# Performance work log

Hardware: AMD Instinct MI355X
Metric: run time of the kernel (lower is better)

## Reference

```python
import jax, jax.numpy as jnp
import numpy as np

N_EMBD = 1024
N_HEAD = 16

def setup_inputs() -> dict:
    key = jax.random.key(0)
    k1, k2, k3, k4, k5 = jax.random.split(key, 5)
    C = N_EMBD
    s = 1.0 / np.sqrt(C)
    return {
        "x": jax.random.normal(k1, (2, 2048, C), dtype=jnp.float32),
        "W_attn": jax.random.normal(k2, (C, 3 * C), dtype=jnp.float32) * s,
        "b_attn": jax.random.normal(k3, (3 * C,), dtype=jnp.float32) * 0.02,
        "W_proj": jax.random.normal(k4, (C, C), dtype=jnp.float32) * s,
        "b_proj": jax.random.normal(k5, (C,), dtype=jnp.float32) * 0.02,
    }

def reference(x, W_attn, b_attn, W_proj, b_proj):
    B, T, C = x.shape
    nh = N_HEAD
    hs = C // nh
    qkv = x @ W_attn + b_attn                      # [B, T, 3C]
    q, k, v = jnp.split(qkv, 3, axis=-1)
    # [B, T, C] -> [B, nh, T, hs]
    def to_heads(t):
        return t.reshape(B, T, nh, hs).transpose(0, 2, 1, 3)
    q, k, v = to_heads(q), to_heads(k), to_heads(v)
    scale = 1.0 / np.sqrt(hs).astype(np.float32)
    att = jnp.einsum('bhqd,bhkd->bhqk', q, k) * scale   # [B, nh, T, T]
    causal = jnp.tril(jnp.ones((T, T), dtype=bool))
    att = jnp.where(causal, att, -jnp.inf)
    att = jax.nn.softmax(att, axis=-1)
    y = jnp.einsum('bhqk,bhkd->bhqd', att, v)           # [B, nh, T, hs]
    y = y.transpose(0, 2, 1, 3).reshape(B, T, C)
    return y @ W_proj + b_proj
```

## Files before the change

kernel.cpp:

```cpp
#include <hip/hip_runtime.h>
#include <hip/hip_bf16.h>
#include <math.h>

#define N_EMBD 1024
#define N_HEAD 16
#define HS 64
#define BT 4096
#define TSEQ 2048

typedef float f32x4 __attribute__((ext_vector_type(4)));
typedef short bf16x8 __attribute__((ext_vector_type(8)));
typedef unsigned short u16;

static __device__ __forceinline__ u16 f2bf(float f) {
  union { float f; unsigned int u; } c; c.f = f;
  unsigned int r = c.u + 0x7FFFu + ((c.u >> 16) & 1u);
  return (u16)(r >> 16);
}

static __device__ __forceinline__ u16 f2bf_fast(float f) {
  union { __hip_bfloat16 h; u16 u; } cv;
  cv.h = __float2bfloat16(f);
  return cv.u;
}

__global__ __launch_bounds__(256) void prep_all(
    const float* __restrict__ x, const float* __restrict__ Wa,
    const float* __restrict__ Wp, u16* __restrict__ xb,
    u16* __restrict__ Wat, u16* __restrict__ Wpt) {
  const int bid = blockIdx.x;
  const int t = threadIdx.x;
  if (bid < 4096) {
    int i = bid * 256 + t;
    float4 v = ((const float4*)x)[i];
    ushort4 o;
    o.x = f2bf(v.x); o.y = f2bf(v.y); o.z = f2bf(v.z); o.w = f2bf(v.w);
    ((ushort4*)xb)[i] = o;
    return;
  }
  __shared__ u16 Ls[32][36];
  const float* W; u16* Wt; int K, N, n0, k0;
  if (bid < 7168) {
    int g = bid - 4096;
    W = Wa; Wt = Wat; K = N_EMBD; N = 3 * N_EMBD;
    n0 = (g % 96) * 32; k0 = (g / 96) * 32;
  } else {
    int g = bid - 7168;
    W = Wp; Wt = Wpt; K = N_EMBD; N = N_EMBD;
    n0 = (g % 32) * 32; k0 = (g / 32) * 32;
  }
  {
    int kk = t >> 3, nn4 = (t & 7) * 4;
    float4 v = *(const float4*)(W + (size_t)(k0 + kk) * N + n0 + nn4);
    Ls[kk][nn4 + 0] = f2bf(v.x); Ls[kk][nn4 + 1] = f2bf(v.y);
    Ls[kk][nn4 + 2] = f2bf(v.z); Ls[kk][nn4 + 3] = f2bf(v.w);
  }
  __syncthreads();
  {
    int nn = t >> 3, kk4 = (t & 7) * 4;
    ushort4 o;
    o.x = Ls[kk4 + 0][nn]; o.y = Ls[kk4 + 1][nn];
    o.z = Ls[kk4 + 2][nn]; o.w = Ls[kk4 + 3][nn];
    *(ushort4*)(Wt + (size_t)(n0 + nn) * K + k0 + kk4) = o;
  }
}

#define BKS 32

__device__ __forceinline__ int swz(int row, int c) {
  return row * 4 + (c ^ ((row >> 1) & 3));
}

__device__ __forceinline__ void stage128x32(const u16* __restrict__ G, int ldk,
                                            u16* lds, int w, int lane) {
#pragma unroll
  for (int i = 0; i < 2; ++i) {
    int s = i * 256 + w * 64 + lane;
    int row = s >> 2, c = s & 3;
    int csrc = c ^ ((row >> 1) & 3);
    const u16* src = G + (size_t)row * ldk + csrc * 8;
    u16* dst = lds + (size_t)(i * 256 + w * 64) * 8;
    __builtin_amdgcn_global_load_lds(
        (const __attribute__((address_space(1))) void*)src,
        (__attribute__((address_space(3))) void*)dst, 16, 0, 0);
  }
}

#define GEMM_MAIN_LOOP(Aptr, Bptr, Kdim)                                        \
  __shared__ u16 sm[2][2][128 * BKS];                                           \
  const int tid = threadIdx.x, lane = tid & 63, w = tid >> 6;                   \
  const int wr = w >> 1, wc = w & 1, lrow = lane & 15, lhi = lane >> 4;         \
  const int _lin = blockIdx.y * gridDim.x + blockIdx.x;                         \
  const int _cpx = (gridDim.x * gridDim.y) >> 3;                                \
  const int _swz = (_lin & 7) * _cpx + (_lin >> 3);                             \
  const int bm = (_swz / gridDim.x) * 128, bn = (_swz % gridDim.x) * 128;       \
  f32x4 acc[4][4];                                                              \
  _Pragma("unroll") for (int i = 0; i < 4; ++i)                                 \
      _Pragma("unroll") for (int j = 0; j < 4; ++j)                             \
          acc[i][j] = (f32x4){0.f, 0.f, 0.f, 0.f};                              \
  stage128x32(Aptr + (size_t)bm * Kdim, Kdim, sm[0][0], w, lane);               \
  stage128x32(Bptr + (size_t)bn * Kdim, Kdim, sm[0][1], w, lane);               \
  __syncthreads();                                                              \
  const int NT = Kdim / BKS;                                                    \
  for (int t = 0; t < NT; ++t) {                                                \
    int cur = t & 1, nxt = cur ^ 1;                                             \
    if (t + 1 < NT) {                                                           \
      stage128x32(Aptr + (size_t)bm * Kdim + (t + 1) * BKS, Kdim, sm[nxt][0],   \
                  w, lane);                                                     \
      stage128x32(Bptr + (size_t)bn * Kdim + (t + 1) * BKS, Kdim, sm[nxt][1],   \
                  w, lane);                                                     \
    }                                                                           \
    const u16* As = sm[cur][0];                                                 \
    const u16* Bs = sm[cur][1];                                                 \
    bf16x8 af[4], bfr[4];                                                       \
    _Pragma("unroll") for (int mi = 0; mi < 4; ++mi) {                          \
      int row = wr * 64 + mi * 16 + lrow;                                       \
      af[mi] = *(const bf16x8*)(As + (size_t)swz(row, lhi) * 8);                \
    }                                                                           \
    _Pragma("unroll") for (int nj = 0; nj < 4; ++nj) {                          \
      int row = wc * 64 + nj * 16 + lrow;                                       \
      bfr[nj] = *(const bf16x8*)(Bs + (size_t)swz(row, lhi) * 8);               \
    }                                                                           \
    _Pragma("unroll") for (int mi = 0; mi < 4; ++mi)                            \
        _Pragma("unroll") for (int nj = 0; nj < 4; ++nj)                        \
            acc[mi][nj] = __builtin_amdgcn_mfma_f32_16x16x32_bf16(              \
                af[mi], bfr[nj], acc[mi][nj], 0, 0, 0);                         \
    __syncthreads();                                                            \
  }

__global__ __launch_bounds__(256) void gemm_qkv_bf16(
    const u16* __restrict__ Ab, const u16* __restrict__ Btr,
    const float* __restrict__ bias,
    u16* __restrict__ Qb, u16* __restrict__ Kb, u16* __restrict__ Vt) {
  GEMM_MAIN_LOOP(Ab, Btr, N_EMBD)
  const int sector = bn >> 10;
  const float QSC = 0.125f * 1.44269504f;
#pragma unroll
  for (int nj = 0; nj < 4; ++nj) {
    int n = bn + wc * 64 + nj * 16 + lrow;
    int h = (n & 1023) >> 6, d = n & 63;
    float bv = bias[n];
#pragma unroll
    for (int mi = 0; mi < 4; ++mi) {
      int mbase = bm + wr * 64 + mi * 16 + lhi * 4;
      int bb_ = mbase >> 11, tt = mbase & 2047;
      if (sector == 0) {
#pragma unroll
        for (int r = 0; r < 4; ++r)
          Qb[((size_t)(bb_ * 16 + h) * TSEQ + tt + r) * HS + d] =
              f2bf((acc[mi][nj][r] + bv) * QSC);
      } else if (sector == 1) {
#pragma unroll
        for (int r = 0; r < 4; ++r)
          Kb[((size_t)(bb_ * 16 + h) * TSEQ + tt + r) * HS + d] =
              f2bf(acc[mi][nj][r] + bv);
      } else {
        ushort4 o;
        o.x = f2bf(acc[mi][nj][0] + bv); o.y = f2bf(acc[mi][nj][1] + bv);
        o.z = f2bf(acc[mi][nj][2] + bv); o.w = f2bf(acc[mi][nj][3] + bv);
        *(ushort4*)(Vt + ((size_t)(bb_ * 16 + h) * HS + d) * TSEQ + tt) = o;
      }
    }
  }
}

__global__ __launch_bounds__(256) void gemm_proj_bf16(
    const u16* __restrict__ Ab, const u16* __restrict__ Btr,
    const float* __restrict__ bias, float* __restrict__ C) {
  GEMM_MAIN_LOOP(Ab, Btr, N_EMBD)
#pragma unroll
  for (int nj = 0; nj < 4; ++nj) {
    int n = bn + wc * 64 + nj * 16 + lrow;
    float bv = bias[n];
#pragma unroll
    for (int mi = 0; mi < 4; ++mi) {
      int mbase = bm + wr * 64 + mi * 16 + lhi * 4;
#pragma unroll
      for (int r = 0; r < 4; ++r)
        C[(size_t)(mbase + r) * N_EMBD + n] = acc[mi][nj][r] + bv;
    }
  }
}

__device__ __forceinline__ void stage_kv(const u16* __restrict__ Kh,
                                         const u16* __restrict__ Vh,
                                         int kb, u16* kbuf, u16* vbuf,
                                         int tid, int w) {
#pragma unroll
  for (int i = 0; i < 2; ++i) {
    int s = i * 256 + tid;
    int r = s >> 3, c = s & 7;
    int cs = c ^ (r & 7);
    const u16* ksrc = Kh + (size_t)(kb + r) * HS + cs * 8;
    u16* kdst = kbuf + (size_t)(i * 256 + (w << 6)) * 8;
    __builtin_amdgcn_global_load_lds(
        (const __attribute__((address_space(1))) void*)ksrc,
        (__attribute__((address_space(3))) void*)kdst, 16, 0, 0);
    const u16* vsrc = Vh + (size_t)r * TSEQ + kb + cs * 8;
    u16* vdst = vbuf + (size_t)(i * 256 + (w << 6)) * 8;
    __builtin_amdgcn_global_load_lds(
        (const __attribute__((address_space(1))) void*)vsrc,
        (__attribute__((address_space(3))) void*)vdst, 16, 0, 0);
  }
}

__global__ __launch_bounds__(256, 2) void attn_part(
    const u16* __restrict__ Qb, const u16* __restrict__ Kb,
    const u16* __restrict__ Vt, u16* __restrict__ Y,
    float* PfLow, float* PfHi, float* __restrict__ Lf) {
  __shared__ u16 Ks[2][64 * HS];
  __shared__ u16 Vs[2][64 * HS];
  __shared__ u16 Plds[4][32][72];

  const int tid  = threadIdx.x;
  const int lane = tid & 63;
  const int w    = tid >> 6;
  const int lrow = lane & 15;
  const int lhi  = lane >> 4;

  const int wg  = blockIdx.x;
  const int xcd = wg & 7;
  const int lin = wg >> 3;
  const int bhl = lin / 34;
  const int id  = lin % 34;
  const int bh  = (xcd << 2) | bhl;
  const int b   = bh >> 4, h = bh & 15;

  int j, part, cnt;
  if (id < 18)      { j = 15 - id / 3;        part = id % 3;        cnt = 3; }
  else if (id < 30) { j = 9 - (id - 18) / 2;  part = (id - 18) & 1; cnt = 2; }
  else              { j = 33 - id;            part = 0;             cnt = 1; }
  const int split  = (cnt > 1);
  const int tsteps = 2 * j + 2;
  const int s0 = (part * tsteps) / cnt;
  const int s1 = ((part + 1) * tsteps) / cnt;
  const int nsteps = s1 - s0;

  const u16* Qh = Qb + (size_t)bh * TSEQ * HS;
  const u16* Kh = Kb + (size_t)bh * TSEQ * HS;
  const u16* Vh = Vt + (size_t)bh * HS * TSEQ;

  const int q0 = j * 128 + w * 32;

  bf16x8 aq[4];
  aq[0] = *(const bf16x8*)(Qh + (size_t)(q0 + lrow) * HS + lhi * 8);
  aq[1] = *(const bf16x8*)(Qh + (size_t)(q0 + lrow) * HS + 32 + lhi * 8);
  aq[2] = *(const bf16x8*)(Qh + (size_t)(q0 + 16 + lrow) * HS + lhi * 8);
  aq[3] = *(const bf16x8*)(Qh + (size_t)(q0 + 16 + lrow) * HS + 32 + lhi * 8);

  bf16x8 ones;
#pragma unroll
  for (int i = 0; i < 8; ++i) ones[i] = (short)0x3F80;

  f32x4 o[2][4], ol[2];
#pragma unroll
  for (int sub = 0; sub < 2; ++sub) {
    ol[sub] = (f32x4){0.f, 0.f, 0.f, 0.f};
#pragma unroll
    for (int ds = 0; ds < 4; ++ds) o[sub][ds] = (f32x4){0.f, 0.f, 0.f, 0.f};
  }

  int kb = s0 * 64;
  stage_kv(Kh, Vh, kb, Ks[0], Vs[0], tid, w);

  for (int t = 0; t < nsteps; ++t) {
    const int cur = t & 1;
    __syncthreads();
    if (t + 1 < nsteps)
      stage_kv(Kh, Vh, kb + 64, Ks[cur ^ 1], Vs[cur ^ 1], tid, w);

    const u16* Kc = Ks[cur];
    const u16* Vc = Vs[cur];

    f32x4 sacc[2][4];
#pragma unroll
    for (int s = 0; s < 4; ++s) {
      int r = s * 16 + lrow;
      bf16x8 k0 = *(const bf16x8*)(Kc + r * HS + ((lhi    ) ^ (r & 7)) * 8);
      bf16x8 k1 = *(const bf16x8*)(Kc + r * HS + ((lhi + 4) ^ (r & 7)) * 8);
      f32x4 z0 = (f32x4){0.f, 0.f, 0.f, 0.f};
      f32x4 z1 = (f32x4){0.f, 0.f, 0.f, 0.f};
      z0 = __builtin_amdgcn_mfma_f32_16x16x32_bf16(aq[0], k0, z0, 0, 0, 0);
      z0 = __builtin_amdgcn_mfma_f32_16x16x32_bf16(aq[1], k1, z0, 0, 0, 0);
      z1 = __builtin_amdgcn_mfma_f32_16x16x32_bf16(aq[2], k0, z1, 0, 0, 0);
      z1 = __builtin_amdgcn_mfma_f32_16x16x32_bf16(aq[3], k1, z1, 0, 0, 0);
      sacc[0][s] = z0; sacc[1][s] = z1;
    }

#pragma unroll
    for (int sub = 0; sub < 2; ++sub) {
      const int qbase = q0 + sub * 16;
      if (kb + 63 > qbase) {
#pragma unroll
        for (int s = 0; s < 4; ++s) {
          int kg = kb + 16 * s + lrow;
#pragma unroll
          for (int r = 0; r < 4; ++r)
            if (kg > qbase + lhi * 4 + r) sacc[sub][s][r] = -3.0e38f;
        }
      }
#pragma unroll
      for (int s = 0; s < 4; ++s)
#pragma unroll
        for (int r = 0; r < 4; ++r)
          Plds[w][sub * 16 + lhi * 4 + r][s * 16 + lrow] =
              f2bf_fast(exp2f(sacc[sub][s][r] - 16.0f));
    }

#pragma unroll
    for (int ks = 0; ks < 2; ++ks) {
      bf16x8 pa0 = *(const bf16x8*)&Plds[w][lrow][ks * 32 + lhi * 8];
      bf16x8 pa1 = *(const bf16x8*)&Plds[w][16 + lrow][ks * 32 + lhi * 8];
      ol[0] = __builtin_amdgcn_mfma_f32_16x16x32_bf16(pa0, ones, ol[0], 0, 0, 0);
      ol[1] = __builtin_amdgcn_mfma_f32_16x16x32_bf16(pa1, ones, ol[1], 0, 0, 0);
#pragma unroll
      for (int ds = 0; ds < 4; ++ds) {
        int vr = ds * 16 + lrow;
        bf16x8 vf = *(const bf16x8*)(Vc + vr * 64 + ((ks * 4 + lhi) ^ (vr & 7)) * 8);
        o[0][ds] = __builtin_amdgcn_mfma_f32_16x16x32_bf16(pa0, vf, o[0][ds], 0, 0, 0);
        o[1][ds] = __builtin_amdgcn_mfma_f32_16x16x32_bf16(pa1, vf, o[1][ds], 0, 0, 0);
      }
    }
    kb += 64;
  }

  if (!split) {
#pragma unroll
    for (int sub = 0; sub < 2; ++sub)
#pragma unroll
      for (int r = 0; r < 4; ++r) {
        float inv = 1.0f / ol[sub][r];
        int q = q0 + sub * 16 + lhi * 4 + r;
#pragma unroll
        for (int ds = 0; ds < 4; ++ds)
          Y[((size_t)(b * TSEQ + q)) * N_EMBD + h * HS + ds * 16 + lrow] =
              f2bf(o[sub][ds][r] * inv);
      }
  } else {
    const int slot = bh * 30 + id;
    float* orow = (slot < 448)
                      ? (PfLow + (size_t)slot * 8192)
                      : (PfHi + (size_t)(slot - 448) * 8192);
#pragma unroll
    for (int sub = 0; sub < 2; ++sub)
#pragma unroll
      for (int r = 0; r < 4; ++r) {
        int row = w * 32 + sub * 16 + lhi * 4 + r;
#pragma unroll
        for (int ds = 0; ds < 4; ++ds)
          orow[row * 64 + ds * 16 + lrow] = o[sub][ds][r];
        if (lrow == 0) Lf[slot * 128 + row] = ol[sub][r];
      }
  }
}

__global__ __launch_bounds__(256) void attn_combine(
    const float* PfLow, const float* PfHi, const float* __restrict__ Lf,
    u16* __restrict__ Y) {
  const int bi = blockIdx.x;
  const int bh = bi / 12, jj = 4 + (bi % 12);
  const int b  = bh >> 4, h = bh & 15;
  int cnt, baseid;
  if (jj >= 10) { cnt = 3; baseid = (15 - jj) * 3; }
  else          { cnt = 2; baseid = 18 + (9 - jj) * 2; }
  const int slot0 = bh * 30 + baseid;

  const int tid = threadIdx.x;
  const int d   = tid & 63;
  const int rg  = tid >> 6;

  for (int rr = 0; rr < 32; ++rr) {
    int row = rg * 32 + rr;
    float l = 0.f, o = 0.f;
    for (int k = 0; k < cnt; ++k) {
      int slot = slot0 + k;
      const float* orow = (slot < 448)
                              ? (PfLow + (size_t)slot * 8192)
                              : (PfHi + (size_t)(slot - 448) * 8192);
      l += Lf[slot * 128 + row];
      o += orow[row * 64 + d];
    }
    int q = jj * 128 + row;
    Y[((size_t)(b * TSEQ + q)) * N_EMBD + h * HS + d] = f2bf(o / l);
  }
}

extern "C" void kernel_launch(void* const* d_in, const int* in_sizes, int n_in,
                              void* d_out, int out_size, void* d_ws, size_t ws_size,
                              hipStream_t stream) {
  const float* x      = (const float*)d_in[0];
  const float* W_attn = (const float*)d_in[1];
  const float* b_attn = (const float*)d_in[2];
  const float* W_proj = (const float*)d_in[3];
  const float* b_proj = (const float*)d_in[4];
  float* out = (float*)d_out;

  u16* xb  = (u16*)d_ws;
  u16* Wat = xb  + (size_t)BT * N_EMBD;
  u16* Wpt = Wat + (size_t)3 * N_EMBD * N_EMBD;
  u16* Qb  = Wpt + (size_t)N_EMBD * N_EMBD;
  u16* Kb  = Qb  + (size_t)BT * N_EMBD;
  u16* Vt  = Kb  + (size_t)BT * N_EMBD;
  u16* yb  = Vt  + (size_t)BT * N_EMBD;
  float* PfLow = (float*)d_ws;
  float* PfHi  = (float*)(yb + (size_t)BT * N_EMBD);
  float* Lf    = PfHi + (size_t)512 * 8192;

  prep_all<<<8192, 256, 0, stream>>>(x, W_attn, W_proj, xb, Wat, Wpt);
  {
    dim3 grid(3 * N_EMBD / 128, BT / 128);
    gemm_qkv_bf16<<<grid, 256, 0, stream>>>(xb, Wat, b_attn, Qb, Kb, Vt);
  }
  {
    attn_part<<<1088, 256, 0, stream>>>(Qb, Kb, Vt, yb, PfLow, PfHi, Lf);
    attn_combine<<<384, 256, 0, stream>>>(PfLow, PfHi, Lf, yb);
  }
  {
    dim3 grid(N_EMBD / 128, BT / 128);
    gemm_proj_bf16<<<grid, 256, 0, stream>>>(yb, Wpt, b_proj, out);
  }
}
```

Baseline: 152.4 us.

## Double attention query tile to 256 rows per block with new split schedule

Each attention workgroup now handles 256 query rows, with 64 per wave, instead of 128. Each K/V tile staged in LDS is therefore reused across twice as many queries, and the block count is halved. The split-K partition table and the combine kernel are rebuilt for 8 query blocks per head, with up to 4 parts for the largest block. The trade-off is more accumulator registers per wave and fewer workgroups, which risks spills or lower occupancy under launch_bounds(256,2) and a coarser load balance.

```diff
diff --git a/kernel.cpp b/kernel.cpp
--- a/kernel.cpp
+++ b/kernel.cpp
@@ -210,7 +210,7 @@
     float* PfLow, float* PfHi, float* __restrict__ Lf) {
   __shared__ u16 Ks[2][64 * HS];
   __shared__ u16 Vs[2][64 * HS];
-  __shared__ u16 Plds[4][32][72];
+  __shared__ u16 Plds[4][64][72];
 
   const int tid  = threadIdx.x;
   const int lane = tid & 63;
@@ -221,17 +221,22 @@
   const int wg  = blockIdx.x;
   const int xcd = wg & 7;
   const int lin = wg >> 3;
-  const int bhl = lin / 34;
-  const int id  = lin % 34;
+  const int bhl = lin / 17;
+  const int id  = lin % 17;
   const int bh  = (xcd << 2) | bhl;
   const int b   = bh >> 4, h = bh & 15;
 
-  int j, part, cnt;
-  if (id < 18)      { j = 15 - id / 3;        part = id % 3;        cnt = 3; }
-  else if (id < 30) { j = 9 - (id - 18) / 2;  part = (id - 18) & 1; cnt = 2; }
-  else              { j = 33 - id;            part = 0;             cnt = 1; }
+  int j, part, cnt, sid;
+  if (id == 0)       { j = 2; part = 0;       cnt = 1; sid = -1; }
+  else if (id <= 2)  { j = 4; part = id - 1;  cnt = 2; sid = id - 1; }
+  else if (id <= 5)  { j = 6; part = id - 3;  cnt = 3; sid = id - 1; }
+  else if (id <= 7)  { j = 3; part = id - 6;  cnt = 2; sid = id - 1; }
+  else if (id <= 11) { j = 7; part = id - 8;  cnt = 4; sid = id - 1; }
+  else if (id <= 14) { j = 5; part = id - 12; cnt = 3; sid = id - 1; }
+  else if (id == 15) { j = 1; part = 0;       cnt = 1; sid = -1; }
+  else               { j = 0; part = 0;       cnt = 1; sid = -1; }
   const int split  = (cnt > 1);
-  const int tsteps = 2 * j + 2;
+  const int tsteps = 4 * j + 4;
   const int s0 = (part * tsteps) / cnt;
   const int s1 = ((part + 1) * tsteps) / cnt;
   const int nsteps = s1 - s0;
@@ -240,21 +245,22 @@
   const u16* Kh = Kb + (size_t)bh * TSEQ * HS;
   const u16* Vh = Vt + (size_t)bh * HS * TSEQ;
 
-  const int q0 = j * 128 + w * 32;
-
-  bf16x8 aq[4];
-  aq[0] = *(const bf16x8*)(Qh + (size_t)(q0 + lrow) * HS + lhi * 8);
-  aq[1] = *(const bf16x8*)(Qh + (size_t)(q0 + lrow) * HS + 32 + lhi * 8);
-  aq[2] = *(const bf16x8*)(Qh + (size_t)(q0 + 16 + lrow) * HS + lhi * 8);
-  aq[3] = *(const bf16x8*)(Qh + (size_t)(q0 + 16 + lrow) * HS + 32 + lhi * 8);
+  const int q0 = j * 256 + w * 64;
+
+  bf16x8 aq[8];
+#pragma unroll
+  for (int sub = 0; sub < 4; ++sub) {
+    aq[2 * sub]     = *(const bf16x8*)(Qh + (size_t)(q0 + sub * 16 + lrow) * HS + lhi * 8);
+    aq[2 * sub + 1] = *(const bf16x8*)(Qh + (size_t)(q0 + sub * 16 + lrow) * HS + 32 + lhi * 8);
+  }
 
   bf16x8 ones;
 #pragma unroll
   for (int i = 0; i < 8; ++i) ones[i] = (short)0x3F80;
 
-  f32x4 o[2][4], ol[2];
-#pragma unroll
-  for (int sub = 0; sub < 2; ++sub) {
+  f32x4 o[4][4], ol[4];
+#pragma unroll
+  for (int sub = 0; sub < 4; ++sub) {
     ol[sub] = (f32x4){0.f, 0.f, 0.f, 0.f};
 #pragma unroll
     for (int ds = 0; ds < 4; ++ds) o[sub][ds] = (f32x4){0.f, 0.f, 0.f, 0.f};
@@ -272,23 +278,23 @@
     const u16* Kc = Ks[cur];
     const u16* Vc = Vs[cur];
 
-    f32x4 sacc[2][4];
+    f32x4 sacc[4][4];
 #pragma unroll
     for (int s = 0; s < 4; ++s) {
       int r = s * 16 + lrow;
       bf16x8 k0 = *(const bf16x8*)(Kc + r * HS + ((lhi    ) ^ (r & 7)) * 8);
       bf16x8 k1 = *(const bf16x8*)(Kc + r * HS + ((lhi + 4) ^ (r & 7)) * 8);
-      f32x4 z0 = (f32x4){0.f, 0.f, 0.f, 0.f};
-      f32x4 z1 = (f32x4){0.f, 0.f, 0.f, 0.f};
-      z0 = __builtin_amdgcn_mfma_f32_16x16x32_bf16(aq[0], k0, z0, 0, 0, 0);
-      z0 = __builtin_amdgcn_mfma_f32_16x16x32_bf16(aq[1], k1, z0, 0, 0, 0);
-      z1 = __builtin_amdgcn_mfma_f32_16x16x32_bf16(aq[2], k0, z1, 0, 0, 0);
-      z1 = __builtin_amdgcn_mfma_f32_16x16x32_bf16(aq[3], k1, z1, 0, 0, 0);
-      sacc[0][s] = z0; sacc[1][s] = z1;
-    }
-
-#pragma unroll
-    for (int sub = 0; sub < 2; ++sub) {
+#pragma unroll
+      for (int sub = 0; sub < 4; ++sub) {
+        f32x4 z = (f32x4){0.f, 0.f, 0.f, 0.f};
+        z = __builtin_amdgcn_mfma_f32_16x16x32_bf16(aq[2 * sub], k0, z, 0, 0, 0);
+        z = __builtin_amdgcn_mfma_f32_16x16x32_bf16(aq[2 * sub + 1], k1, z, 0, 0, 0);
+        sacc[sub][s] = z;
+      }
+    }
+
+#pragma unroll
+    for (int sub = 0; sub < 4; ++sub) {
       const int qbase = q0 + sub * 16;
       if (kb + 63 > qbase) {
 #pragma unroll
@@ -309,16 +315,20 @@
 
 #pragma unroll
     for (int ks = 0; ks < 2; ++ks) {
-      bf16x8 pa0 = *(const bf16x8*)&Plds[w][lrow][ks * 32 + lhi * 8];
-      bf16x8 pa1 = *(const bf16x8*)&Plds[w][16 + lrow][ks * 32 + lhi * 8];
-      ol[0] = __builtin_amdgcn_mfma_f32_16x16x32_bf16(pa0, ones, ol[0], 0, 0, 0);
-      ol[1] = __builtin_amdgcn_mfma_f32_16x16x32_bf16(pa1, ones, ol[1], 0, 0, 0);
+      bf16x8 pa[4];
+#pragma unroll
+      for (int sub = 0; sub < 4; ++sub)
+        pa[sub] = *(const bf16x8*)&Plds[w][sub * 16 + lrow][ks * 32 + lhi * 8];
+#pragma unroll
+      for (int sub = 0; sub < 4; ++sub)
+        ol[sub] = __builtin_amdgcn_mfma_f32_16x16x32_bf16(pa[sub], ones, ol[sub], 0, 0, 0);
 #pragma unroll
       for (int ds = 0; ds < 4; ++ds) {
         int vr = ds * 16 + lrow;
         bf16x8 vf = *(const bf16x8*)(Vc + vr * 64 + ((ks * 4 + lhi) ^ (vr & 7)) * 8);
-        o[0][ds] = __builtin_amdgcn_mfma_f32_16x16x32_bf16(pa0, vf, o[0][ds], 0, 0, 0);
-        o[1][ds] = __builtin_amdgcn_mfma_f32_16x16x32_bf16(pa1, vf, o[1][ds], 0, 0, 0);
+#pragma unroll
+        for (int sub = 0; sub < 4; ++sub)
+          o[sub][ds] = __builtin_amdgcn_mfma_f32_16x16x32_bf16(pa[sub], vf, o[sub][ds], 0, 0, 0);
       }
     }
     kb += 64;
@@ -326,7 +336,7 @@
 
   if (!split) {
 #pragma unroll
-    for (int sub = 0; sub < 2; ++sub)
+    for (int sub = 0; sub < 4; ++sub)
 #pragma unroll
       for (int r = 0; r < 4; ++r) {
         float inv = 1.0f / ol[sub][r];
@@ -337,19 +347,19 @@
               f2bf(o[sub][ds][r] * inv);
       }
   } else {
-    const int slot = bh * 30 + id;
-    float* orow = (slot < 448)
-                      ? (PfLow + (size_t)slot * 8192)
-                      : (PfHi + (size_t)(slot - 448) * 8192);
-#pragma unroll
-    for (int sub = 0; sub < 2; ++sub)
+    const int slot = bh * 14 + sid;
+    float* orow = (slot < 224)
+                      ? (PfLow + (size_t)slot * 16384)
+                      : (PfHi + (size_t)(slot - 224) * 16384);
+#pragma unroll
+    for (int sub = 0; sub < 4; ++sub)
 #pragma unroll
       for (int r = 0; r < 4; ++r) {
-        int row = w * 32 + sub * 16 + lhi * 4 + r;
+        int row = w * 64 + sub * 16 + lhi * 4 + r;
 #pragma unroll
         for (int ds = 0; ds < 4; ++ds)
           orow[row * 64 + ds * 16 + lrow] = o[sub][ds][r];
-        if (lrow == 0) Lf[slot * 128 + row] = ol[sub][r];
+        if (lrow == 0) Lf[slot * 256 + row] = ol[sub][r];
       }
   }
 }
@@ -358,29 +368,32 @@
     const float* PfLow, const float* PfHi, const float* __restrict__ Lf,
     u16* __restrict__ Y) {
   const int bi = blockIdx.x;
-  const int bh = bi / 12, jj = 4 + (bi % 12);
+  const int bh = bi / 5, u = bi % 5;
   const int b  = bh >> 4, h = bh & 15;
-  int cnt, baseid;
-  if (jj >= 10) { cnt = 3; baseid = (15 - jj) * 3; }
-  else          { cnt = 2; baseid = 18 + (9 - jj) * 2; }
-  const int slot0 = bh * 30 + baseid;
+  int j, base, cnt;
+  if (u == 0)      { j = 3; base = 5;  cnt = 2; }
+  else if (u == 1) { j = 4; base = 0;  cnt = 2; }
+  else if (u == 2) { j = 5; base = 11; cnt = 3; }
+  else if (u == 3) { j = 6; base = 2;  cnt = 3; }
+  else             { j = 7; base = 7;  cnt = 4; }
+  const int slot0 = bh * 14 + base;
 
   const int tid = threadIdx.x;
   const int d   = tid & 63;
   const int rg  = tid >> 6;
 
-  for (int rr = 0; rr < 32; ++rr) {
-    int row = rg * 32 + rr;
+  for (int rr = 0; rr < 64; ++rr) {
+    int row = rg * 64 + rr;
     float l = 0.f, o = 0.f;
     for (int k = 0; k < cnt; ++k) {
       int slot = slot0 + k;
-      const float* orow = (slot < 448)
-                              ? (PfLow + (size_t)slot * 8192)
-                              : (PfHi + (size_t)(slot - 448) * 8192);
-      l += Lf[slot * 128 + row];
+      const float* orow = (slot < 224)
+                              ? (PfLow + (size_t)slot * 16384)
+                              : (PfHi + (size_t)(slot - 224) * 16384);
+      l += Lf[slot * 256 + row];
       o += orow[row * 64 + d];
     }
-    int q = jj * 128 + row;
+    int q = j * 256 + row;
     Y[((size_t)(b * TSEQ + q)) * N_EMBD + h * HS + d] = f2bf(o / l);
   }
 }
@@ -404,7 +417,7 @@
   u16* yb  = Vt  + (size_t)BT * N_EMBD;
   float* PfLow = (float*)d_ws;
   float* PfHi  = (float*)(yb + (size_t)BT * N_EMBD);
-  float* Lf    = PfHi + (size_t)512 * 8192;
+  float* Lf    = PfHi + (size_t)224 * 16384;
 
   prep_all<<<8192, 256, 0, stream>>>(x, W_attn, W_proj, xb, Wat, Wpt);
   {
@@ -412,8 +425,8 @@
     gemm_qkv_bf16<<<grid, 256, 0, stream>>>(xb, Wat, b_attn, Qb, Kb, Vt);
   }
   {
-    attn_part<<<1088, 256, 0, stream>>>(Qb, Kb, Vt, yb, PfLow, PfHi, Lf);
-    attn_combine<<<384, 256, 0, stream>>>(PfLow, PfHi, Lf, yb);
+    attn_part<<<544, 256, 0, stream>>>(Qb, Kb, Vt, yb, PfLow, PfHi, Lf);
+    attn_combine<<<160, 256, 0, stream>>>(PfLow, PfHi, Lf, yb);
   }
   {
     dim3 grid(N_EMBD / 128, BT / 128);
```

After: 202.4 us. +32.8%, slower.
